# Kernel tuning notes

Hardware: AMD Instinct MI355X
Metric: run time of the kernel (lower is better)

## Reference

```python
import jax, jax.numpy as jnp
import numpy as np

B = 16384          # batch
F = 64             # number of feature columns (tables)
L = 10             # pooled lookups per feature (bag size)
E = 16             # embedding dim
V = 1_000_000      # hashed vocab size (shared table)
D = F * E          # concat width = 1024
EPS = 1e-5


def setup_inputs() -> dict:
    key = jax.random.key(0)
    ks = jax.random.split(key, 9)
    idx = jax.random.randint(ks[0], (B, F, L), 0, V, dtype=jnp.int64)
    # NormalTensorInitializer(var=0.01) -> std 0.1
    emb = jax.random.normal(ks[1], (V, E), dtype=jnp.float32) * 0.1
    W1 = jax.random.normal(ks[2], (D, 1024), dtype=jnp.float32) / np.sqrt(D).astype(np.float32)
    b1 = jnp.zeros((1024,), jnp.float32)
    W2 = jax.random.normal(ks[3], (1024, 512), dtype=jnp.float32) / np.sqrt(1024).astype(np.float32)
    b2 = jnp.zeros((512,), jnp.float32)
    W3 = jax.random.normal(ks[4], (512, 1), dtype=jnp.float32) / np.sqrt(512).astype(np.float32)
    b3 = jnp.zeros((1,), jnp.float32)
    return {"idx": idx, "emb": emb, "W1": W1, "b1": b1,
            "W2": W2, "b2": b2, "W3": W3, "b3": b3}


def reference(idx, emb, W1, b1, W2, b2, W3, b3):
    # EmbeddingSumConcat: gather [B,F,L,E], sum-pool over bag dim, concat features
    pooled = jnp.take(emb, idx, axis=0).sum(axis=2)          # [B, F, E]
    x = pooled.reshape(B, D)                                  # [B, F*E]
    # ms.nn.Normalization: per-feature batch standardization
    mu = x.mean(axis=0, keepdims=True)
    var = x.var(axis=0, keepdims=True)
    x = (x - mu) * jax.lax.rsqrt(var + EPS)
    # Dense tower 1024 -> 1024 -> 512 -> 1, sigmoid
    h = jax.nn.relu(x @ W1 + b1)
    h = jax.nn.relu(h @ W2 + b2)
    out = jax.nn.sigmoid(h @ W3 + b3)                         # [B, 1]
    return out
```

## Files before the change

kernel.cpp:

```cpp
#include <hip/hip_runtime.h>
#include <hip/hip_bf16.h>
#include <math.h>

typedef __attribute__((ext_vector_type(8))) short  short8;
typedef __attribute__((ext_vector_type(4))) float  f32x4;
typedef __attribute__((ext_vector_type(4))) unsigned short u16x4;
typedef __attribute__((ext_vector_type(8))) unsigned short u16x8;

#define BATCH 16384
#define NF    64
#define BAGL  10
#define ED    16
#define DW    1024
#define VOCAB 1000000

static __device__ __forceinline__ unsigned short f2bf(float f) {
    unsigned int u = __builtin_bit_cast(unsigned int, f);
    unsigned int r = (u + 0x7fffu + ((u >> 16) & 1u)) >> 16;
    return (unsigned short)r;
}
static __device__ __forceinline__ float bf2f(unsigned short h) {
    unsigned int u = ((unsigned int)h) << 16;
    return __builtin_bit_cast(float, u);
}

__global__ __launch_bounds__(256) void emb_to_bf16(const float* __restrict__ e,
                                                   unsigned short* __restrict__ o) {
    const long long i = ((long long)blockIdx.x * 256 + threadIdx.x) * 8;
    if (i >= (long long)VOCAB * ED) return;
    const f32x4 a = *(const f32x4*)(e + i);
    const f32x4 b = *(const f32x4*)(e + i + 4);
    u16x8 r;
#pragma unroll
    for (int j = 0; j < 4; ++j) { r[j] = f2bf(a[j]); r[4 + j] = f2bf(b[j]); }
    *(u16x8*)(o + i) = r;
}

__global__ __launch_bounds__(256) void pool_bf16(const int* __restrict__ idx,
                                                 const unsigned short* __restrict__ embb,
                                                 unsigned short* __restrict__ xb) {
    const int gid = blockIdx.x * 256 + threadIdx.x;
    const int bag = gid >> 1;
    const int h   = gid & 1;
    const int* ip = idx + (long long)bag * BAGL;

    int v[BAGL];
#pragma unroll
    for (int l = 0; l < BAGL; ++l) v[l] = ip[l];
    u16x8 e[BAGL];
#pragma unroll
    for (int l = 0; l < BAGL; ++l)
        e[l] = *(const u16x8*)(embb + (((long long)v[l]) << 4) + h * 8);

    float s[8] = {0, 0, 0, 0, 0, 0, 0, 0};
#pragma unroll
    for (int l = 0; l < BAGL; ++l)
#pragma unroll
        for (int j = 0; j < 8; ++j) s[j] += bf2f(e[l][j]);

    u16x8 o;
#pragma unroll
    for (int j = 0; j < 8; ++j) o[j] = f2bf(s[j]);
    *(u16x8*)(xb + (((long long)bag) << 4) + h * 8) = o;
}

__global__ __launch_bounds__(256) void stats_kernel(const unsigned short* __restrict__ xb,
                                                    float* __restrict__ ssum,
                                                    float* __restrict__ ssq) {
    const int t = threadIdx.x;
    const long long r0 = (long long)blockIdx.x * 128;
    float s[4] = {0, 0, 0, 0}, q[4] = {0, 0, 0, 0};
    for (int r = 0; r < 128; ++r) {
        const u16x4 v = *(const u16x4*)(xb + (r0 + r) * DW + t * 4);
#pragma unroll
        for (int j = 0; j < 4; ++j) { float f = bf2f(v[j]); s[j] += f; q[j] += f * f; }
    }
#pragma unroll
    for (int j = 0; j < 4; ++j) {
        atomicAdd(&ssum[t * 4 + j], s[j]);
        atomicAdd(&ssq [t * 4 + j], q[j]);
    }
}

__global__ void finalize_stats(const float* __restrict__ ssum, const float* __restrict__ ssq,
                               float* __restrict__ mean, float* __restrict__ rsig,
                               float* __restrict__ murs) {
    const int c = blockIdx.x * 256 + threadIdx.x;
    const float m = ssum[c] * (1.0f / (float)BATCH);
    const float v = ssq[c] * (1.0f / (float)BATCH) - m * m;
    const float r = rsqrtf(v + 1e-5f);
    mean[c] = m; rsig[c] = r; murs[c] = m * r;
}

template <int SCALE>
__global__ __launch_bounds__(256) void transpose_f32_bf16(const float* __restrict__ src,
                                                          unsigned short* __restrict__ dst,
                                                          int R, int C,
                                                          const float* __restrict__ rs) {
    __shared__ float tile[32][33];
    const int tx = threadIdx.x & 31, ty = threadIdx.x >> 5;
    const int bx = blockIdx.x, by = blockIdx.y;
#pragma unroll
    for (int i = 0; i < 4; ++i) {
        const int r = by * 32 + ty + i * 8, c = bx * 32 + tx;
        float v = src[(long long)r * C + c];
        if (SCALE) v *= rs[r];
        tile[ty + i * 8][tx] = v;
    }
    __syncthreads();
#pragma unroll
    for (int i = 0; i < 4; ++i) {
        const int oc = bx * 32 + ty + i * 8;
        dst[(long long)oc * R + by * 32 + tx] = f2bf(tile[tx][ty + i * 8]);
    }
}

__global__ __launch_bounds__(256) void b1fold_kernel(const float* __restrict__ W1,
                                                     const float* __restrict__ murs,
                                                     float* __restrict__ b1n) {
    const int n = blockIdx.x * 256 + threadIdx.x;
    const int k0 = blockIdx.y * 128;
    float acc = 0.f;
#pragma unroll 4
    for (int k = 0; k < 128; ++k)
        acc += murs[k0 + k] * W1[(long long)(k0 + k) * 1024 + n];
    atomicAdd(&b1n[n], -acc);
}

__global__ __launch_bounds__(256) void gemm_relu(const unsigned short* __restrict__ A,
                                                 const unsigned short* __restrict__ Bt,
                                                 const float* __restrict__ bias,
                                                 const float* __restrict__ bias2,
                                                 unsigned short* __restrict__ C,
                                                 int M, int N, int K, int NBN) {
    __shared__ __align__(16) unsigned short As[128 * 64];
    __shared__ __align__(16) unsigned short Bs[128 * 64];
    const int tid = threadIdx.x;
    const int w = tid >> 6, l = tid & 63;
    const int wr = w >> 1, wc = w & 1;
    const int blk = blockIdx.x, xcd = blk & 7, j = blk >> 3;
    const int bm = xcd * 16 + j / NBN, bn = j % NBN;
    const int l15 = l & 15, l4 = l >> 4;

    f32x4 acc[4][4] = {};
    const long long a_base = (long long)bm * 128 * K;
    const long long b_base = (long long)bn * 128 * K;

    for (int k0 = 0; k0 < K; k0 += 64) {
#pragma unroll
        for (int i = 0; i < 4; ++i) {
            const int cid = i * 256 + tid;
            const int row = cid >> 3, kq = (cid & 7) << 3;
            __builtin_amdgcn_global_load_lds(
                (const __attribute__((address_space(1))) void*)(A + a_base + (long long)row * K + k0 + kq),
                (__attribute__((address_space(3))) void*)(&As[cid * 8]), 16, 0, 0);
            __builtin_amdgcn_global_load_lds(
                (const __attribute__((address_space(1))) void*)(Bt + b_base + (long long)row * K + k0 + kq),
                (__attribute__((address_space(3))) void*)(&Bs[cid * 8]), 16, 0, 0);
        }
        __syncthreads();

        short8 a[2][4], b[2][4];
#pragma unroll
        for (int kk = 0; kk < 2; ++kk) {
#pragma unroll
            for (int m = 0; m < 4; ++m)
                a[kk][m] = *(const short8*)(As + (wr * 64 + m * 16 + l15) * 64 + kk * 32 + l4 * 8);
#pragma unroll
            for (int n = 0; n < 4; ++n)
                b[kk][n] = *(const short8*)(Bs + (wc * 64 + n * 16 + l15) * 64 + kk * 32 + l4 * 8);
        }
#pragma unroll
        for (int kk = 0; kk < 2; ++kk)
#pragma unroll
            for (int m = 0; m < 4; ++m)
#pragma unroll
                for (int n = 0; n < 4; ++n)
                    acc[m][n] = __builtin_amdgcn_mfma_f32_16x16x32_bf16(a[kk][m], b[kk][n], acc[m][n], 0, 0, 0);
        __syncthreads();
    }

#pragma unroll
    for (int m = 0; m < 4; ++m) {
        const int grow_base = bm * 128 + wr * 64 + m * 16 + l4 * 4;
#pragma unroll
        for (int n = 0; n < 4; ++n) {
            const int gcol = bn * 128 + wc * 64 + n * 16 + l15;
            const float bv = bias[gcol] + (bias2 ? bias2[gcol] : 0.f);
#pragma unroll
            for (int j2 = 0; j2 < 4; ++j2) {
                float v = fmaxf(acc[m][n][j2] + bv, 0.f);
                C[(long long)(grow_base + j2) * N + gcol] = f2bf(v);
            }
        }
    }
}

__global__ __launch_bounds__(256) void gemm2_fused(const unsigned short* __restrict__ A,
                                                   const unsigned short* __restrict__ Bt,
                                                   const float* __restrict__ bias,
                                                   const float* __restrict__ W3,
                                                   float* __restrict__ logits,
                                                   int M, int N, int K, int NBN) {
    __shared__ __align__(16) unsigned short As[128 * 64];
    __shared__ __align__(16) unsigned short Bs[128 * 64];
    const int tid = threadIdx.x;
    const int w = tid >> 6, l = tid & 63;
    const int wr = w >> 1, wc = w & 1;
    const int blk = blockIdx.x, xcd = blk & 7, j = blk >> 3;
    const int bm = xcd * 16 + j / NBN, bn = j % NBN;
    const int l15 = l & 15, l4 = l >> 4;

    f32x4 acc[4][4] = {};
    const long long a_base = (long long)bm * 128 * K;
    const long long b_base = (long long)bn * 128 * K;

    for (int k0 = 0; k0 < K; k0 += 64) {
#pragma unroll
        for (int i = 0; i < 4; ++i) {
            const int cid = i * 256 + tid;
            const int row = cid >> 3, kq = (cid & 7) << 3;
            __builtin_amdgcn_global_load_lds(
                (const __attribute__((address_space(1))) void*)(A + a_base + (long long)row * K + k0 + kq),
                (__attribute__((address_space(3))) void*)(&As[cid * 8]), 16, 0, 0);
            __builtin_amdgcn_global_load_lds(
                (const __attribute__((address_space(1))) void*)(Bt + b_base + (long long)row * K + k0 + kq),
                (__attribute__((address_space(3))) void*)(&Bs[cid * 8]), 16, 0, 0);
        }
        __syncthreads();

        short8 a[2][4], b[2][4];
#pragma unroll
        for (int kk = 0; kk < 2; ++kk) {
#pragma unroll
            for (int m = 0; m < 4; ++m)
                a[kk][m] = *(const short8*)(As + (wr * 64 + m * 16 + l15) * 64 + kk * 32 + l4 * 8);
#pragma unroll
            for (int n = 0; n < 4; ++n)
                b[kk][n] = *(const short8*)(Bs + (wc * 64 + n * 16 + l15) * 64 + kk * 32 + l4 * 8);
        }
#pragma unroll
        for (int kk = 0; kk < 2; ++kk)
#pragma unroll
            for (int m = 0; m < 4; ++m)
#pragma unroll
                for (int n = 0; n < 4; ++n)
                    acc[m][n] = __builtin_amdgcn_mfma_f32_16x16x32_bf16(a[kk][m], b[kk][n], acc[m][n], 0, 0, 0);
        __syncthreads();
    }

#pragma unroll
    for (int m = 0; m < 4; ++m) {
        float part[4] = {0.f, 0.f, 0.f, 0.f};
#pragma unroll
        for (int n = 0; n < 4; ++n) {
            const int gcol = bn * 128 + wc * 64 + n * 16 + l15;
            const float bv = bias[gcol];
            const float w3 = W3[gcol];
#pragma unroll
            for (int j2 = 0; j2 < 4; ++j2) {
                float v = fmaxf(acc[m][n][j2] + bv, 0.f);
                part[j2] += v * w3;
            }
        }
#pragma unroll
        for (int off = 1; off < 16; off <<= 1)
#pragma unroll
            for (int j2 = 0; j2 < 4; ++j2) part[j2] += __shfl_xor(part[j2], off, 64);
        if (l15 == 0) {
            const int grow = bm * 128 + wr * 64 + m * 16 + l4 * 4;
#pragma unroll
            for (int j2 = 0; j2 < 4; ++j2) atomicAdd(&logits[grow + j2], part[j2]);
        }
    }
}

__global__ __launch_bounds__(256) void sigmoid_kernel(const float* __restrict__ logits,
                                                      const float* __restrict__ b3,
                                                      float* __restrict__ out) {
    const int i = blockIdx.x * 256 + threadIdx.x;
    out[i] = 1.0f / (1.0f + expf(-(logits[i] + b3[0])));
}

extern "C" void kernel_launch(void* const* d_in, const int* in_sizes, int n_in,
                              void* d_out, int out_size, void* d_ws, size_t ws_size,
                              hipStream_t stream) {
    const int*   idx = (const int*)d_in[0];
    const float* emb = (const float*)d_in[1];
    const float* W1  = (const float*)d_in[2];
    const float* b1  = (const float*)d_in[3];
    const float* W2  = (const float*)d_in[4];
    const float* b2  = (const float*)d_in[5];
    const float* W3  = (const float*)d_in[6];
    const float* b3  = (const float*)d_in[7];
    float* out = (float*)d_out;

    const size_t EMBB_H1_BYTES = (size_t)BATCH * DW * 2;

    char* ws = (char*)d_ws;
    unsigned short* xb   = (unsigned short*)ws; ws += (size_t)BATCH * DW * 2;
    unsigned short* embb = (unsigned short*)ws; ws += EMBB_H1_BYTES;
    unsigned short* h1   = embb;
    unsigned short* w1t  = (unsigned short*)ws; ws += (size_t)1024 * 1024 * 2;
    unsigned short* w2t  = (unsigned short*)ws; ws += (size_t)512 * 1024 * 2;
    float* ssum   = (float*)ws; ws += 4096;
    float* ssq    = (float*)ws; ws += 4096;
    float* b1n    = (float*)ws; ws += 4096;
    float* logits = (float*)ws; ws += (size_t)BATCH * 4;
    float* mean   = (float*)ws; ws += 4096;
    float* rsig   = (float*)ws; ws += 4096;
    float* murs   = (float*)ws; ws += 4096;

    hipMemsetAsync(ssum, 0, 4096 * 3 + (size_t)BATCH * 4, stream);

    const long long embElems = (long long)VOCAB * ED;
    const int embBlocks = (int)((embElems / 8 + 255) / 256);
    emb_to_bf16<<<embBlocks, 256, 0, stream>>>(emb, embb);
    pool_bf16<<<(BATCH * NF * 2) / 256, 256, 0, stream>>>(idx, embb, xb);
    stats_kernel<<<BATCH / 128, 256, 0, stream>>>(xb, ssum, ssq);
    finalize_stats<<<4, 256, 0, stream>>>(ssum, ssq, mean, rsig, murs);

    transpose_f32_bf16<1><<<dim3(32, 32), 256, 0, stream>>>(W1, w1t, 1024, 1024, rsig);
    b1fold_kernel<<<dim3(4, 8), 256, 0, stream>>>(W1, murs, b1n);
    transpose_f32_bf16<0><<<dim3(16, 32), 256, 0, stream>>>(W2, w2t, 1024, 512, nullptr);

    gemm_relu<<<(BATCH / 128) * (1024 / 128), 256, 0, stream>>>(
        xb, w1t, b1, b1n, h1, BATCH, 1024, 1024, 1024 / 128);
    gemm2_fused<<<(BATCH / 128) * (512 / 128), 256, 0, stream>>>(
        h1, w2t, b2, W3, logits, BATCH, 512, 1024, 512 / 128);

    sigmoid_kernel<<<BATCH / 256, 256, 0, stream>>>(logits, b3, out);
}
```

Before: 325.8 us.

## Pool directly from fp32 table; double-buffer swizzled GEMMs with larger GEMM1 tiles

```diff
diff --git a/kernel.cpp b/kernel.cpp
--- a/kernel.cpp
+++ b/kernel.cpp
@@ -24,44 +24,30 @@
     return __builtin_bit_cast(float, u);
 }
 
-__global__ __launch_bounds__(256) void emb_to_bf16(const float* __restrict__ e,
-                                                   unsigned short* __restrict__ o) {
-    const long long i = ((long long)blockIdx.x * 256 + threadIdx.x) * 8;
-    if (i >= (long long)VOCAB * ED) return;
-    const f32x4 a = *(const f32x4*)(e + i);
-    const f32x4 b = *(const f32x4*)(e + i + 4);
-    u16x8 r;
-#pragma unroll
-    for (int j = 0; j < 4; ++j) { r[j] = f2bf(a[j]); r[4 + j] = f2bf(b[j]); }
-    *(u16x8*)(o + i) = r;
-}
-
-__global__ __launch_bounds__(256) void pool_bf16(const int* __restrict__ idx,
-                                                 const unsigned short* __restrict__ embb,
-                                                 unsigned short* __restrict__ xb) {
+__global__ __launch_bounds__(256) void pool_kernel(const int* __restrict__ idx,
+                                                   const float* __restrict__ emb,
+                                                   unsigned short* __restrict__ xb) {
     const int gid = blockIdx.x * 256 + threadIdx.x;
-    const int bag = gid >> 1;
-    const int h   = gid & 1;
+    const int bag = gid >> 2;
+    const int q   = gid & 3;
     const int* ip = idx + (long long)bag * BAGL;
 
     int v[BAGL];
 #pragma unroll
     for (int l = 0; l < BAGL; ++l) v[l] = ip[l];
-    u16x8 e[BAGL];
+    f32x4 e[BAGL];
 #pragma unroll
     for (int l = 0; l < BAGL; ++l)
-        e[l] = *(const u16x8*)(embb + (((long long)v[l]) << 4) + h * 8);
-
-    float s[8] = {0, 0, 0, 0, 0, 0, 0, 0};
-#pragma unroll
-    for (int l = 0; l < BAGL; ++l)
-#pragma unroll
-        for (int j = 0; j < 8; ++j) s[j] += bf2f(e[l][j]);
-
-    u16x8 o;
-#pragma unroll
-    for (int j = 0; j < 8; ++j) o[j] = f2bf(s[j]);
-    *(u16x8*)(xb + (((long long)bag) << 4) + h * 8) = o;
+        e[l] = *(const f32x4*)(emb + (((long long)v[l]) << 4) + (q << 2));
+
+    f32x4 s01 = e[0] + e[1], s23 = e[2] + e[3], s45 = e[4] + e[5],
+          s67 = e[6] + e[7], s89 = e[8] + e[9];
+    f32x4 acc = ((s01 + s23) + (s45 + s67)) + s89;
+
+    u16x4 o;
+#pragma unroll
+    for (int j = 0; j < 4; ++j) o[j] = f2bf(acc[j]);
+    *(u16x4*)(xb + (((long long)bag) << 4) + (q << 2)) = o;
 }
 
 __global__ __launch_bounds__(256) void stats_kernel(const unsigned short* __restrict__ xb,
@@ -127,66 +113,109 @@
     atomicAdd(&b1n[n], -acc);
 }
 
-__global__ __launch_bounds__(256) void gemm_relu(const unsigned short* __restrict__ A,
-                                                 const unsigned short* __restrict__ Bt,
-                                                 const float* __restrict__ bias,
-                                                 const float* __restrict__ bias2,
-                                                 unsigned short* __restrict__ C,
-                                                 int M, int N, int K, int NBN) {
-    __shared__ __align__(16) unsigned short As[128 * 64];
-    __shared__ __align__(16) unsigned short Bs[128 * 64];
+__global__ __launch_bounds__(512, 2) void gemm1_256(const unsigned short* __restrict__ A,
+                                                    const unsigned short* __restrict__ Bt,
+                                                    const float* __restrict__ bias,
+                                                    const float* __restrict__ bias2,
+                                                    unsigned short* __restrict__ C,
+                                                    int M, int N, int K) {
+    __shared__ __align__(16) unsigned short As[2][256 * 64];
+    __shared__ __align__(16) unsigned short Bs[2][256 * 64];
     const int tid = threadIdx.x;
     const int w = tid >> 6, l = tid & 63;
-    const int wr = w >> 1, wc = w & 1;
-    const int blk = blockIdx.x, xcd = blk & 7, j = blk >> 3;
-    const int bm = xcd * 16 + j / NBN, bn = j % NBN;
+    const int wr = w >> 2, wc = w & 3;
     const int l15 = l & 15, l4 = l >> 4;
-
-    f32x4 acc[4][4] = {};
-    const long long a_base = (long long)bm * 128 * K;
-    const long long b_base = (long long)bn * 128 * K;
-
-    for (int k0 = 0; k0 < K; k0 += 64) {
-#pragma unroll
-        for (int i = 0; i < 4; ++i) {
-            const int cid = i * 256 + tid;
-            const int row = cid >> 3, kq = (cid & 7) << 3;
-            __builtin_amdgcn_global_load_lds(
-                (const __attribute__((address_space(1))) void*)(A + a_base + (long long)row * K + k0 + kq),
-                (__attribute__((address_space(3))) void*)(&As[cid * 8]), 16, 0, 0);
-            __builtin_amdgcn_global_load_lds(
-                (const __attribute__((address_space(1))) void*)(Bt + b_base + (long long)row * K + k0 + kq),
-                (__attribute__((address_space(3))) void*)(&Bs[cid * 8]), 16, 0, 0);
-        }
-        __syncthreads();
-
-        short8 a[2][4], b[2][4];
-#pragma unroll
-        for (int kk = 0; kk < 2; ++kk) {
-#pragma unroll
-            for (int m = 0; m < 4; ++m)
-                a[kk][m] = *(const short8*)(As + (wr * 64 + m * 16 + l15) * 64 + kk * 32 + l4 * 8);
-#pragma unroll
-            for (int n = 0; n < 4; ++n)
-                b[kk][n] = *(const short8*)(Bs + (wc * 64 + n * 16 + l15) * 64 + kk * 32 + l4 * 8);
-        }
-#pragma unroll
-        for (int kk = 0; kk < 2; ++kk)
-#pragma unroll
-            for (int m = 0; m < 4; ++m)
-#pragma unroll
-                for (int n = 0; n < 4; ++n)
-                    acc[m][n] = __builtin_amdgcn_mfma_f32_16x16x32_bf16(a[kk][m], b[kk][n], acc[m][n], 0, 0, 0);
-        __syncthreads();
-    }
-
-#pragma unroll
-    for (int m = 0; m < 4; ++m) {
-        const int grow_base = bm * 128 + wr * 64 + m * 16 + l4 * 4;
+    const int blk = blockIdx.x, xcd = blk & 7, jj = blk >> 3;
+    const int bm = xcd * 8 + (jj >> 2), bn = jj & 3;
+
+    f32x4 acc[8][4] = {};
+    const long long a_base = (long long)bm * 256 * K;
+    const long long b_base = (long long)bn * 256 * K;
+    const int NT = K >> 6;
+
+#define G1_STAGE(buf, kt)                                                       \
+  {                                                                             \
+    const int k0s = (kt) * 64;                                                  \
+    _Pragma("unroll")                                                           \
+    for (int g = 0; g < 4; ++g) {                                               \
+      const int cid = g * 512 + tid;                                            \
+      const int rr = cid >> 3, pos = cid & 7;                                   \
+      const int csrc = (pos ^ (rr & 7)) << 3;                                   \
+      __builtin_amdgcn_global_load_lds(                                         \
+        (const __attribute__((address_space(1))) void*)(A + a_base + (long long)rr * K + k0s + csrc), \
+        (__attribute__((address_space(3))) void*)(&As[buf][cid * 8]), 16, 0, 0);\
+      __builtin_amdgcn_global_load_lds(                                         \
+        (const __attribute__((address_space(1))) void*)(Bt + b_base + (long long)rr * K + k0s + csrc), \
+        (__attribute__((address_space(3))) void*)(&Bs[buf][cid * 8]), 16, 0, 0);\
+    }                                                                           \
+  }
+
+    G1_STAGE(0, 0)
+    G1_STAGE(1, 1)
+    asm volatile("s_waitcnt vmcnt(8)" ::: "memory");
+    __builtin_amdgcn_sched_barrier(0);
+    __builtin_amdgcn_s_barrier();
+
+    for (int t = 0; t < NT; ++t) {
+        const unsigned short* Ap = As[t & 1];
+        const unsigned short* Bp = Bs[t & 1];
+        short8 a[8], b[4];
+
+        {
+            const int swz = ((0 * 4 + l4) ^ (l15 & 7)) << 3;
+#pragma unroll
+            for (int m = 0; m < 8; ++m)
+                a[m] = *(const short8*)(Ap + (wr * 128 + m * 16 + l15) * 64 + swz);
+#pragma unroll
+            for (int n = 0; n < 4; ++n)
+                b[n] = *(const short8*)(Bp + (wc * 64 + n * 16 + l15) * 64 + swz);
+        }
+        asm volatile("s_waitcnt lgkmcnt(0)" ::: "memory");
+        __builtin_amdgcn_sched_barrier(0);
+        __builtin_amdgcn_s_setprio(1);
+#pragma unroll
+        for (int m = 0; m < 8; ++m)
+#pragma unroll
+            for (int n = 0; n < 4; ++n)
+                acc[m][n] = __builtin_amdgcn_mfma_f32_16x16x32_bf16(a[m], b[n], acc[m][n], 0, 0, 0);
+        __builtin_amdgcn_s_setprio(0);
+
+        {
+            const int swz = ((1 * 4 + l4) ^ (l15 & 7)) << 3;
+#pragma unroll
+            for (int m = 0; m < 8; ++m)
+                a[m] = *(const short8*)(Ap + (wr * 128 + m * 16 + l15) * 64 + swz);
+#pragma unroll
+            for (int n = 0; n < 4; ++n)
+                b[n] = *(const short8*)(Bp + (wc * 64 + n * 16 + l15) * 64 + swz);
+        }
+        asm volatile("s_waitcnt lgkmcnt(0)" ::: "memory");
+        __builtin_amdgcn_sched_barrier(0);
+        __builtin_amdgcn_s_barrier();
+        if (t + 2 < NT) { G1_STAGE((t & 1), t + 2) }
+        __builtin_amdgcn_s_setprio(1);
+#pragma unroll
+        for (int m = 0; m < 8; ++m)
+#pragma unroll
+            for (int n = 0; n < 4; ++n)
+                acc[m][n] = __builtin_amdgcn_mfma_f32_16x16x32_bf16(a[m], b[n], acc[m][n], 0, 0, 0);
+        __builtin_amdgcn_s_setprio(0);
+        if (t + 1 < NT) {
+            if (t + 2 < NT) { asm volatile("s_waitcnt vmcnt(8)" ::: "memory"); }
+            else            { asm volatile("s_waitcnt vmcnt(0)" ::: "memory"); }
+            __builtin_amdgcn_sched_barrier(0);
+            __builtin_amdgcn_s_barrier();
+        }
+    }
+#undef G1_STAGE
+
+#pragma unroll
+    for (int m = 0; m < 8; ++m) {
+        const int grow_base = bm * 256 + wr * 128 + m * 16 + l4 * 4;
 #pragma unroll
         for (int n = 0; n < 4; ++n) {
-            const int gcol = bn * 128 + wc * 64 + n * 16 + l15;
-            const float bv = bias[gcol] + (bias2 ? bias2[gcol] : 0.f);
+            const int gcol = bn * 256 + wc * 64 + n * 16 + l15;
+            const float bv = bias[gcol] + bias2[gcol];
 #pragma unroll
             for (int j2 = 0; j2 < 4; ++j2) {
                 float v = fmaxf(acc[m][n][j2] + bv, 0.f);
@@ -196,49 +225,67 @@
     }
 }
 
-__global__ __launch_bounds__(256) void gemm2_fused(const unsigned short* __restrict__ A,
-                                                   const unsigned short* __restrict__ Bt,
-                                                   const float* __restrict__ bias,
-                                                   const float* __restrict__ W3,
-                                                   float* __restrict__ logits,
-                                                   int M, int N, int K, int NBN) {
-    __shared__ __align__(16) unsigned short As[128 * 64];
-    __shared__ __align__(16) unsigned short Bs[128 * 64];
+#define GEMM_STAGE(dstA, dstB, kt)                                              \
+  {                                                                             \
+    const int k0s = (kt) * 64;                                                  \
+    _Pragma("unroll")                                                           \
+    for (int g = 0; g < 4; ++g) {                                               \
+      const int cid = g * 256 + tid;                                            \
+      const int rr = cid >> 3, pos = cid & 7;                                   \
+      const int csrc = (pos ^ (rr & 7)) << 3;                                   \
+      __builtin_amdgcn_global_load_lds(                                         \
+        (const __attribute__((address_space(1))) void*)(A + a_base + (long long)rr * K + k0s + csrc), \
+        (__attribute__((address_space(3))) void*)(&(dstA)[cid * 8]), 16, 0, 0); \
+      __builtin_amdgcn_global_load_lds(                                         \
+        (const __attribute__((address_space(1))) void*)(Bt + b_base + (long long)rr * K + k0s + csrc), \
+        (__attribute__((address_space(3))) void*)(&(dstB)[cid * 8]), 16, 0, 0); \
+    }                                                                           \
+  }
+
+__global__ __launch_bounds__(256, 2) void gemm2_fused(const unsigned short* __restrict__ A,
+                                                      const unsigned short* __restrict__ Bt,
+                                                      const float* __restrict__ bias,
+                                                      const float* __restrict__ W3,
+                                                      float* __restrict__ logits,
+                                                      int M, int N, int K, int NBN) {
+    __shared__ __align__(16) unsigned short As[2][128 * 64];
+    __shared__ __align__(16) unsigned short Bs[2][128 * 64];
     const int tid = threadIdx.x;
     const int w = tid >> 6, l = tid & 63;
     const int wr = w >> 1, wc = w & 1;
+    const int l15 = l & 15, l4 = l >> 4;
     const int blk = blockIdx.x, xcd = blk & 7, j = blk >> 3;
     const int bm = xcd * 16 + j / NBN, bn = j % NBN;
-    const int l15 = l & 15, l4 = l >> 4;
 
     f32x4 acc[4][4] = {};
     const long long a_base = (long long)bm * 128 * K;
     const long long b_base = (long long)bn * 128 * K;
-
-    for (int k0 = 0; k0 < K; k0 += 64) {
-#pragma unroll
-        for (int i = 0; i < 4; ++i) {
-            const int cid = i * 256 + tid;
-            const int row = cid >> 3, kq = (cid & 7) << 3;
-            __builtin_amdgcn_global_load_lds(
-                (const __attribute__((address_space(1))) void*)(A + a_base + (long long)row * K + k0 + kq),
-                (__attribute__((address_space(3))) void*)(&As[cid * 8]), 16, 0, 0);
-            __builtin_amdgcn_global_load_lds(
-                (const __attribute__((address_space(1))) void*)(Bt + b_base + (long long)row * K + k0 + kq),
-                (__attribute__((address_space(3))) void*)(&Bs[cid * 8]), 16, 0, 0);
-        }
-        __syncthreads();
-
+    const int NT = K >> 6;
+
+    GEMM_STAGE(As[0], Bs[0], 0)
+    GEMM_STAGE(As[1], Bs[1], 1)
+    asm volatile("s_waitcnt vmcnt(8)" ::: "memory");
+    __builtin_amdgcn_sched_barrier(0);
+    __builtin_amdgcn_s_barrier();
+    for (int t = 0; t < NT; ++t) {
+        const unsigned short* Ap = As[t & 1];
+        const unsigned short* Bp = Bs[t & 1];
         short8 a[2][4], b[2][4];
 #pragma unroll
         for (int kk = 0; kk < 2; ++kk) {
+            const int swz = ((kk * 4 + l4) ^ (l15 & 7)) << 3;
 #pragma unroll
             for (int m = 0; m < 4; ++m)
-                a[kk][m] = *(const short8*)(As + (wr * 64 + m * 16 + l15) * 64 + kk * 32 + l4 * 8);
-#pragma unroll
-            for (int n = 0; n < 4; ++n)
-                b[kk][n] = *(const short8*)(Bs + (wc * 64 + n * 16 + l15) * 64 + kk * 32 + l4 * 8);
-        }
+                a[kk][m] = *(const short8*)(Ap + (wr * 64 + m * 16 + l15) * 64 + swz);
+#pragma unroll
+            for (int n = 0; n < 4; ++n)
+                b[kk][n] = *(const short8*)(Bp + (wc * 64 + n * 16 + l15) * 64 + swz);
+        }
+        asm volatile("s_waitcnt lgkmcnt(0)" ::: "memory");
+        __builtin_amdgcn_sched_barrier(0);
+        __builtin_amdgcn_s_barrier();
+        if (t + 2 < NT) { GEMM_STAGE(As[t & 1], Bs[t & 1], t + 2) }
+        __builtin_amdgcn_s_setprio(1);
 #pragma unroll
         for (int kk = 0; kk < 2; ++kk)
 #pragma unroll
@@ -246,7 +293,13 @@
 #pragma unroll
                 for (int n = 0; n < 4; ++n)
                     acc[m][n] = __builtin_amdgcn_mfma_f32_16x16x32_bf16(a[kk][m], b[kk][n], acc[m][n], 0, 0, 0);
-        __syncthreads();
+        __builtin_amdgcn_s_setprio(0);
+        if (t + 1 < NT) {
+            if (t + 2 < NT) { asm volatile("s_waitcnt vmcnt(8)" ::: "memory"); }
+            else            { asm volatile("s_waitcnt vmcnt(0)" ::: "memory"); }
+            __builtin_amdgcn_sched_barrier(0);
+            __builtin_amdgcn_s_barrier();
+        }
     }
 
 #pragma unroll
@@ -295,12 +348,9 @@
     const float* b3  = (const float*)d_in[7];
     float* out = (float*)d_out;
 
-    const size_t EMBB_H1_BYTES = (size_t)BATCH * DW * 2;
-
     char* ws = (char*)d_ws;
     unsigned short* xb   = (unsigned short*)ws; ws += (size_t)BATCH * DW * 2;
-    unsigned short* embb = (unsigned short*)ws; ws += EMBB_H1_BYTES;
-    unsigned short* h1   = embb;
+    unsigned short* h1   = (unsigned short*)ws; ws += (size_t)BATCH * DW * 2;
     unsigned short* w1t  = (unsigned short*)ws; ws += (size_t)1024 * 1024 * 2;
     unsigned short* w2t  = (unsigned short*)ws; ws += (size_t)512 * 1024 * 2;
     float* ssum   = (float*)ws; ws += 4096;
@@ -313,10 +363,7 @@
 
     hipMemsetAsync(ssum, 0, 4096 * 3 + (size_t)BATCH * 4, stream);
 
-    const long long embElems = (long long)VOCAB * ED;
-    const int embBlocks = (int)((embElems / 8 + 255) / 256);
-    emb_to_bf16<<<embBlocks, 256, 0, stream>>>(emb, embb);
-    pool_bf16<<<(BATCH * NF * 2) / 256, 256, 0, stream>>>(idx, embb, xb);
+    pool_kernel<<<(BATCH * NF * 4) / 256, 256, 0, stream>>>(idx, emb, xb);
     stats_kernel<<<BATCH / 128, 256, 0, stream>>>(xb, ssum, ssq);
     finalize_stats<<<4, 256, 0, stream>>>(ssum, ssq, mean, rsig, murs);
 
@@ -324,8 +371,8 @@
     b1fold_kernel<<<dim3(4, 8), 256, 0, stream>>>(W1, murs, b1n);
     transpose_f32_bf16<0><<<dim3(16, 32), 256, 0, stream>>>(W2, w2t, 1024, 512, nullptr);
 
-    gemm_relu<<<(BATCH / 128) * (1024 / 128), 256, 0, stream>>>(
-        xb, w1t, b1, b1n, h1, BATCH, 1024, 1024, 1024 / 128);
+    gemm1_256<<<(BATCH / 256) * (1024 / 256), 512, 0, stream>>>(
+        xb, w1t, b1, b1n, h1, BATCH, 1024, 1024);
     gemm2_fused<<<(BATCH / 128) * (512 / 128), 256, 0, stream>>>(
         h1, w2t, b2, W3, logits, BATCH, 512, 1024, 512 / 128);
 
```

Result: faster. 296.9 us (-8.9%).
